# Kernel optimization log

Measured on AMD Instinct MI355X. Metric: run time of the kernel, lower is better.

## Reference

```python
import jax, jax.numpy as jnp
import numpy as np

D_MODEL = 1024
NHEAD = 16
HEAD_DIM = D_MODEL // NHEAD
FF = 4096
ALPHA = 1.4142135  # deepnorm_alpha
WIN = (127, 128)   # sliding window (left, right)
EPS = 1e-5
ROPE_BASE = 10000.0


def rmsnorm(x, g):
    ms = jnp.mean(x * x, axis=-1, keepdims=True)
    return x * jax.lax.rsqrt(ms + EPS) * g


def rope(x):
    # x: [B, T, H, D]; non-interleaved rotary over full head dim
    T, D = x.shape[1], x.shape[-1]
    half = D // 2
    inv_freq = 1.0 / (ROPE_BASE ** (jnp.arange(half, dtype=jnp.float32) * 2.0 / D))
    ang = jnp.arange(T, dtype=jnp.float32)[:, None] * inv_freq[None, :]  # [T, half]
    cos = jnp.cos(ang)[None, :, None, :]
    sin = jnp.sin(ang)[None, :, None, :]
    x1, x2 = x[..., :half], x[..., half:]
    return jnp.concatenate([x1 * cos - x2 * sin, x2 * cos + x1 * sin], axis=-1)


def setup_inputs() -> dict:
    key = jax.random.key(0)
    ks = jax.random.split(key, 8)
    d, h = D_MODEL, FF
    return {
        "x": jax.random.normal(ks[0], (2, 2048, d), jnp.float32),
        "Wqkv": jax.random.normal(ks[1], (3 * d, d), jnp.float32) * 0.02,
        "Wout": jax.random.normal(ks[2], (d, d), jnp.float32) * 0.02,
        "bout": jnp.zeros((d,), jnp.float32),
        "W1": jax.random.normal(ks[3], (2 * h, d), jnp.float32) * 0.02,
        "W2": jax.random.normal(ks[4], (d, h), jnp.float32) * 0.02,
        "g1": jnp.ones((d,), jnp.float32),
        "g2": jnp.ones((d,), jnp.float32),
    }


def reference(x, Wqkv, Wout, bout, W1, W2, g1, g2):
    B, T, d = x.shape
    # --- self attention with RoPE + sliding window band mask ---
    qkv = (x @ Wqkv.T).reshape(B, T, 3, NHEAD, HEAD_DIM)
    q, k, v = qkv[:, :, 0], qkv[:, :, 1], qkv[:, :, 2]  # [B,T,H,Dh]
    q = rope(q)
    k = rope(k)
    q = jnp.swapaxes(q, 1, 2)  # [B,H,T,Dh]
    k = jnp.swapaxes(k, 1, 2)
    v = jnp.swapaxes(v, 1, 2)
    scale = 1.0 / np.sqrt(HEAD_DIM)
    scores = jnp.einsum('bhqd,bhkd->bhqk', q, k) * scale
    idx = jnp.arange(T)
    rel = idx[None, :] - idx[:, None]  # j - i
    band = (rel >= -WIN[0]) & (rel <= WIN[1])  # [T,T] allowed positions
    scores = jnp.where(band[None, None], scores, -jnp.inf)
    attn = jax.nn.softmax(scores, axis=-1)
    o = jnp.einsum('bhqk,bhkd->bhqd', attn, v)
    o = jnp.swapaxes(o, 1, 2).reshape(B, T, d)
    a = o @ Wout.T + bout
    # --- deepnorm residual 1 + RMSNorm ---
    x1 = a + ALPHA * x
    x2 = rmsnorm(x1, g1)
    # --- SwiGLU MLP: y, gate = fc1(x).chunk(2); y*gate*sigmoid(gate) ---
    yg = x2 @ W1.T
    y, gate = jnp.split(yg, 2, axis=-1)
    y = y * gate * jax.nn.sigmoid(gate)
    y = y @ W2.T
    # --- deepnorm residual 2 + RMSNorm ---
    x3 = y + ALPHA * x2
    return rmsnorm(x3, g2)
```

## Files before the change

### kernel.cpp

```cpp
#include <hip/hip_runtime.h>

#define T_SEQ   2048
#define NHEADS  16
#define DHEAD   64
#define DMODEL  1024
#define ALPHA_C 1.4142135f
#define EPS_C   1e-5f

typedef __attribute__((ext_vector_type(8))) short bf16x8;
typedef __attribute__((ext_vector_type(4))) short bf16x4;
typedef __attribute__((ext_vector_type(4))) float floatx4;

__device__ __forceinline__ float bf2f(unsigned short u) {
  union { unsigned int i; float f; } v;
  v.i = ((unsigned int)u) << 16;
  return v.f;
}
__device__ __forceinline__ unsigned short f2bf(float f) {
  union { float f; unsigned int i; } v;
  v.f = f;
  unsigned int u = v.i;
  u += 0x7FFF + ((u >> 16) & 1);
  return (unsigned short)(u >> 16);
}

__device__ __forceinline__ void gload_lds16(const void* g, void* l) {
  __builtin_amdgcn_global_load_lds(
      (const __attribute__((address_space(1))) void*)g,
      (__attribute__((address_space(3))) void*)l, 16, 0, 0);
}

__global__ void convert_all(const float* __restrict__ Wqkv,
                            const float* __restrict__ Wout,
                            const float* __restrict__ W1,
                            const float* __restrict__ W2,
                            const float* __restrict__ x,
                            unsigned short* __restrict__ ws)
{
  size_t i = ((size_t)blockIdx.x * 256 + threadIdx.x) * 8;
  const float* src;
  size_t off;
  if      (i <  3145728) { src = Wqkv; off = i; }
  else if (i <  4194304) { src = Wout; off = i -  3145728; }
  else if (i < 12582912) { src = W1;   off = i -  4194304; }
  else if (i < 16777216) { src = W2;   off = i - 12582912; }
  else                   { src = x;    off = i - 16777216; }
  floatx4 a = *(const floatx4*)(src + off);
  floatx4 b = *(const floatx4*)(src + off + 4);
  bf16x8 o;
  #pragma unroll
  for (int u = 0; u < 4; u++) {
    o[u]     = (short)f2bf(a[u]);
    o[4 + u] = (short)f2bf(b[u]);
  }
  *(bf16x8*)(ws + i) = o;
}

__global__ void build_rope_lut(float* __restrict__ cosT,
                               float* __restrict__ sinT)
{
  int gid = blockIdx.x * 256 + threadIdx.x;
  int t = gid >> 5, i = gid & 31;
  float fr = powf(10000.f, -(float)i * (1.f / 32.f));
  float sn, cs;
  sincosf((float)t * fr, &sn, &cs);
  cosT[gid] = cs;
  sinT[gid] = sn;
}

template<int BN>
__global__ __launch_bounds__(256) void gemm_lds(
    const unsigned short* __restrict__ A,
    const unsigned short* __restrict__ W,
    unsigned short* __restrict__ C,
    const float* __restrict__ bias,
    int M, int N, int K, int lda)
{
  constexpr int WN = BN / 2;
  constexpr int NJ = WN / 16;
  __shared__ unsigned short As[128 * 32];
  __shared__ unsigned short Bs[BN * 32];

  const int tid  = threadIdx.x;
  const int lane = tid & 63;
  const int wave = tid >> 6;
  const int wm = (wave >> 1) * 64;
  const int wn = (wave & 1) * WN;
  const int mBase = blockIdx.y * 128;
  const int nBase = blockIdx.x * BN;

  const int sRow = lane >> 2;
  const int sCol = (lane & 3) * 8;

  floatx4 acc[4][NJ];
  #pragma unroll
  for (int i = 0; i < 4; i++)
    #pragma unroll
    for (int j = 0; j < NJ; j++) acc[i][j] = (floatx4){0.f, 0.f, 0.f, 0.f};

  const int mrow = lane & 15;
  const int kq   = (lane >> 4) * 8;

  for (int kb = 0; kb < K; kb += 32) {
    __syncthreads();
    #pragma unroll
    for (int j = 0; j < 2; j++) {
      int r = wave * 32 + j * 16 + sRow;
      gload_lds16(A + (size_t)(mBase + r) * lda + kb + sCol,
                  &As[wave * 1024 + j * 512 + lane * 8]);
    }
    if constexpr (BN == 128) {
      #pragma unroll
      for (int j = 0; j < 2; j++) {
        int r = wave * 32 + j * 16 + sRow;
        gload_lds16(W + (size_t)(nBase + r) * K + kb + sCol,
                    &Bs[wave * 1024 + j * 512 + lane * 8]);
      }
    } else {
      int r = wave * 16 + sRow;
      gload_lds16(W + (size_t)(nBase + r) * K + kb + sCol,
                  &Bs[wave * 512 + lane * 8]);
    }
    __syncthreads();

    bf16x8 af[4], bfr[NJ];
    #pragma unroll
    for (int i = 0; i < 4; i++)
      af[i] = *(const bf16x8*)&As[(wm + i * 16 + mrow) * 32 + kq];
    #pragma unroll
    for (int j = 0; j < NJ; j++)
      bfr[j] = *(const bf16x8*)&Bs[(wn + j * 16 + mrow) * 32 + kq];
    #pragma unroll
    for (int i = 0; i < 4; i++)
      #pragma unroll
      for (int j = 0; j < NJ; j++)
        acc[i][j] = __builtin_amdgcn_mfma_f32_16x16x32_bf16(af[i], bfr[j], acc[i][j], 0, 0, 0);
  }

  const int col0 = lane & 15;
  const int row0 = (lane >> 4) * 4;
  #pragma unroll
  for (int j = 0; j < NJ; j++) {
    const int col = nBase + wn + j * 16 + col0;
    const float badd = bias ? bias[col] : 0.f;
    #pragma unroll
    for (int i = 0; i < 4; i++) {
      #pragma unroll
      for (int r = 0; r < 4; r++) {
        const int row = mBase + wm + i * 16 + row0 + r;
        C[(size_t)row * N + col] = f2bf(acc[i][j][r] + badd);
      }
    }
  }
}

#define BAR() __builtin_amdgcn_s_barrier()
#define SCB() __builtin_amdgcn_sched_barrier(0)
#define LGKM0() do { asm volatile("s_waitcnt lgkmcnt(0)" ::: "memory"); \
                     __builtin_amdgcn_sched_barrier(0); } while (0)

#define RD_A(bb, mh)                                                      \
  _Pragma("unroll") for (int i = 0; i < 4; i++)                           \
  _Pragma("unroll") for (int s = 0; s < 2; s++)                           \
    af[i][s] = *(const bf16x8*)&lds[(bb) + aRd +                          \
        ((mh) * 64 + i * 16 + mrow) * 64 + (kq0 ^ (s << 5))];

#define RD_B(bb, nh)                                                      \
  _Pragma("unroll") for (int n = 0; n < 2; n++)                           \
  _Pragma("unroll") for (int s = 0; s < 2; s++)                           \
    bf[(nh) * 2 + n][s] = *(const bf16x8*)&lds[(bb) + bRd +               \
        (bRow0 + ((nh) * 2 + n) * 16 + mrow) * 64 + (kq0 ^ (s << 5))];

#define MFMA16(mh, nh)                                                    \
  _Pragma("unroll") for (int i = 0; i < 4; i++)                           \
  _Pragma("unroll") for (int n = 0; n < 2; n++)                           \
  _Pragma("unroll") for (int s = 0; s < 2; s++)                           \
    acc[(mh) * 4 + i][(nh) * 2 + n] =                                     \
        __builtin_amdgcn_mfma_f32_16x16x32_bf16(                          \
            af[i][s], bf[(nh) * 2 + n][s],                                \
            acc[(mh) * 4 + i][(nh) * 2 + n], 0, 0, 0);

#define KLOOP_4PH()                                                       \
  for (int t = 0; t < 16; ++t) {                                          \
    const int cur = t & 1;                                                \
    const int nxt = cur ^ 1;                                              \
    const int bb  = cur * 32768;                                          \
    const int ta  = (t + 1 < 16) ? t + 1 : 15;                            \
    const int tb  = (t + 2 < 16) ? t + 2 : 15;                            \
                                       \
    RD_A(bb, 0); RD_B(bb, 0);                                             \
    stA(nxt, 1, ta);                                                      \
    BAR(); LGKM0();                                                       \
    __builtin_amdgcn_s_setprio(1);                                        \
    MFMA16(0, 0);                                                         \
    __builtin_amdgcn_s_setprio(0);                                        \
    BAR();                                                                \
                                                     \
    RD_B(bb, 1);                                                          \
    stB(nxt, 1, ta);                                                      \
    BAR(); LGKM0();                                                       \
    __builtin_amdgcn_s_setprio(1);                                        \
    MFMA16(0, 1);                                                         \
    __builtin_amdgcn_s_setprio(0);                                        \
    BAR();                                                                \
                                                     \
    RD_A(bb, 1);                                                          \
    stB(cur, 0, tb);                                                      \
    BAR(); LGKM0();                                                       \
    __builtin_amdgcn_s_setprio(1);                                        \
    MFMA16(1, 1);                                                         \
    __builtin_amdgcn_s_setprio(0);                                        \
    BAR();                                                                \
       \
    stA(cur, 0, tb);                                                      \
    BAR(); LGKM0();                                                       \
    __builtin_amdgcn_s_setprio(1);                                        \
    MFMA16(1, 0);                                                         \
    __builtin_amdgcn_s_setprio(0);                                        \
    asm volatile("s_waitcnt vmcnt(4)" ::: "memory");                      \
    BAR();                                                                \
  }

__global__ __launch_bounds__(512, 2) void gemm_w1_swiglu_4ph(
    const unsigned short* __restrict__ A,
    const unsigned short* __restrict__ W1,
    unsigned short* __restrict__ ys)
{
  __shared__ unsigned short lds[65536];

  const int tid  = threadIdx.x;
  const int lane = tid & 63;
  const int wid  = tid >> 6;
  const int wr   = wid >> 2;
  const int wc   = wid & 3;
  const int mrow = lane & 15;
  const int quad = lane >> 4;
  const int kq0  = (quad ^ (mrow & 7)) * 8;

  const int bid  = blockIdx.x;
  const int c8   = bid & 7;
  const int u    = bid >> 3;
  const int mBase = ((c8 >> 2) * 8 + (u >> 3)) * 256;
  const int nBase = ((c8 &  3) * 8 + (u &  7)) * 128;

  const int r0 = tid >> 3;
  const int ce = (((tid & 7) ^ (r0 & 7)) * 8);
  const size_t aoff0 = (size_t)(mBase + r0) * 1024 + ce;
  const size_t aoff1 = aoff0 + (size_t)64 * 1024;
  auto growf = [&](int br) {
    int col = nBase + (br >> 6) * 32 + (br & 31);
    return ((br >> 5) & 1) ? 4096 + col : col;
  };
  const size_t boff00 = (size_t)growf(r0)       * 1024 + ce;
  const size_t boff01 = (size_t)growf(64 + r0)  * 1024 + ce;
  const size_t boff10 = (size_t)growf(128 + r0) * 1024 + ce;
  const size_t boff11 = (size_t)growf(192 + r0) * 1024 + ce;
  const int d0 = tid * 8;

  auto stA = [&](int buf, int h, int kt) {
    const unsigned short* g = A + (size_t)kt * 64 + (h ? (size_t)128 * 1024 : 0);
    int base = buf * 32768 + h * 8192;
    gload_lds16(g + aoff0, &lds[base + d0]);
    gload_lds16(g + aoff1, &lds[base + 4096 + d0]);
  };
  auto stB = [&](int buf, int h, int kt) {
    const unsigned short* g = W1 + (size_t)kt * 64;
    int base = buf * 32768 + 16384 + h * 8192;
    gload_lds16(g + (h ? boff10 : boff00), &lds[base + d0]);
    gload_lds16(g + (h ? boff11 : boff01), &lds[base + 4096 + d0]);
  };

  floatx4 acc[8][4];
  #pragma unroll
  for (int i = 0; i < 8; i++)
    #pragma unroll
    for (int n = 0; n < 4; n++) acc[i][n] = (floatx4){0.f, 0.f, 0.f, 0.f};
  bf16x8 af[4][2], bf[4][2];

  const int aRd   = wr * 8192;
  const int bRd   = 16384 + (wc >> 1) * 8192;
  const int bRow0 = (wc & 1) * 64;

  stB(0, 0, 0); stA(0, 0, 0); stA(0, 1, 0); stB(0, 1, 0);
  stB(1, 0, 1); stA(1, 0, 1);
  asm volatile("s_waitcnt vmcnt(4)" ::: "memory");
  BAR();

  KLOOP_4PH();

  const int col0 = lane & 15;
  const int row0 = (lane >> 4) * 4;
  #pragma unroll
  for (int n = 0; n < 2; n++) {
    const int col = nBase + wc * 32 + n * 16 + col0;
    #pragma unroll
    for (int i = 0; i < 8; i++) {
      const int rowb = mBase + wr * 128 + i * 16 + row0;
      #pragma unroll
      for (int r = 0; r < 4; r++) {
        float y = acc[i][n][r], g = acc[i][n + 2][r];
        float sig = 1.f / (1.f + __expf(-g));
        ys[(size_t)(rowb + r) * 4096 + col] = f2bf(y * g * sig);
      }
    }
  }
  asm volatile("s_waitcnt vmcnt(0)" ::: "memory");
}

__global__ __launch_bounds__(512, 2) void gemm_qkv_rope256(
    const unsigned short* __restrict__ A,
    const unsigned short* __restrict__ W,
    const float* __restrict__ cosT,
    const float* __restrict__ sinT,
    unsigned short* __restrict__ Qd,
    unsigned short* __restrict__ Kd,
    unsigned short* __restrict__ Vd)
{
  __shared__ unsigned short lds[65536];

  const int tid  = threadIdx.x;
  const int lane = tid & 63;
  const int wid  = tid >> 6;
  const int wr   = wid >> 2;
  const int wc   = wid & 3;
  const int mrow = lane & 15;
  const int quad = lane >> 4;
  const int kq0  = (quad ^ (mrow & 7)) * 8;

  const int bid  = blockIdx.x;
  const int c8   = bid & 7;
  const int u    = bid >> 3;
  const int mBase = ((c8 >> 1) * 4 + u / 6) * 256;
  const int nBase = ((c8 & 1) * 6 + u % 6) * 256;

  const int r0 = tid >> 3;
  const int ce = (((tid & 7) ^ (r0 & 7)) * 8);
  const size_t aoff0 = (size_t)(mBase + r0) * 1024 + ce;
  const size_t aoff1 = aoff0 + (size_t)64 * 1024;
  const size_t boff00 = (size_t)(nBase + r0)       * 1024 + ce;
  const size_t boff01 = (size_t)(nBase + 64 + r0)  * 1024 + ce;
  const size_t boff10 = (size_t)(nBase + 128 + r0) * 1024 + ce;
  const size_t boff11 = (size_t)(nBase + 192 + r0) * 1024 + ce;
  const int d0 = tid * 8;

  auto stA = [&](int buf, int h, int kt) {
    const unsigned short* g = A + (size_t)kt * 64 + (h ? (size_t)128 * 1024 : 0);
    int base = buf * 32768 + h * 8192;
    gload_lds16(g + aoff0, &lds[base + d0]);
    gload_lds16(g + aoff1, &lds[base + 4096 + d0]);
  };
  auto stB = [&](int buf, int h, int kt) {
    const unsigned short* g = W + (size_t)kt * 64;
    int base = buf * 32768 + 16384 + h * 8192;
    gload_lds16(g + (h ? boff10 : boff00), &lds[base + d0]);
    gload_lds16(g + (h ? boff11 : boff01), &lds[base + 4096 + d0]);
  };

  floatx4 acc[8][4];
  #pragma unroll
  for (int i = 0; i < 8; i++)
    #pragma unroll
    for (int n = 0; n < 4; n++) acc[i][n] = (floatx4){0.f, 0.f, 0.f, 0.f};
  bf16x8 af[4][2], bf[4][2];

  const int aRd   = wr * 8192;
  const int bRd   = 16384 + (wc >> 1) * 8192;
  const int bRow0 = (wc & 1) * 64;

  stB(0, 0, 0); stA(0, 0, 0); stA(0, 1, 0); stB(0, 1, 0);
  stB(1, 0, 1); stA(1, 0, 1);
  asm volatile("s_waitcnt vmcnt(4)" ::: "memory");
  BAR();

  KLOOP_4PH();

  const int col0 = lane & 15;
  const int row0 = (lane >> 4) * 4;
  const int colBase = nBase + wc * 64;
  const int sect = colBase >> 10;
  const int h    = (colBase & 1023) >> 6;
  unsigned short* dst = (sect == 0) ? Qd : (sect == 1) ? Kd : Vd;

  if (sect < 2) {
    #pragma unroll
    for (int i = 0; i < 8; i++) {
      #pragma unroll
      for (int r = 0; r < 4; r++) {
        const int row = mBase + wr * 128 + i * 16 + row0 + r;
        const int b = row >> 11, t = row & 2047;
        size_t ob = ((size_t)((b * NHEADS + h) * T_SEQ + t)) * DHEAD;
        const int tb = t * 32;
        float c0 = cosT[tb + col0],      s0 = sinT[tb + col0];
        float c1 = cosT[tb + col0 + 16], s1 = sinT[tb + col0 + 16];
        float x1a = acc[i][0][r], x2a = acc[i][2][r];
        float x1b = acc[i][1][r], x2b = acc[i][3][r];
        dst[ob + col0]      = f2bf(x1a * c0 - x2a * s0);
        dst[ob + col0 + 32] = f2bf(x2a * c0 + x1a * s0);
        dst[ob + col0 + 16] = f2bf(x1b * c1 - x2b * s1);
        dst[ob + col0 + 48] = f2bf(x2b * c1 + x1b * s1);
      }
    }
  } else {
    #pragma unroll
    for (int i = 0; i < 8; i++)
      #pragma unroll
      for (int n = 0; n < 4; n++)
        #pragma unroll
        for (int r = 0; r < 4; r++) {
          const int row = mBase + wr * 128 + i * 16 + row0 + r;
          const int b = row >> 11, t = row & 2047;
          dst[((size_t)((b * NHEADS + h) * T_SEQ + t)) * DHEAD + n * 16 + col0] =
              f2bf(acc[i][n][r]);
        }
  }
  asm volatile("s_waitcnt vmcnt(0)" ::: "memory");
}

#define W2_RD_A(bb, mh, s)                                                \
  _Pragma("unroll") for (int i = 0; i < 2; i++)                           \
    af[i][s] = *(const bf16x8*)&lds[(bb) +                                \
        (wr * 64 + (mh) * 32 + i * 16 + mrow) * 64 + (kq0 ^ ((s) << 5))];

#define W2_RD_B(bb, s)                                                    \
  _Pragma("unroll") for (int n = 0; n < 4; n++)                           \
    bfr[n][s] = *(const bf16x8*)&lds[(bb) + 16384 +                       \
        (wc * 64 + n * 16 + mrow) * 64 + (kq0 ^ ((s) << 5))];

#define W2_MFMA(mh, s)                                                    \
  _Pragma("unroll") for (int i = 0; i < 2; i++)                           \
  _Pragma("unroll") for (int n = 0; n < 4; n++)                           \
    acc[(mh) * 2 + i][n] =                                                \
        __builtin_amdgcn_mfma_f32_16x16x32_bf16(                          \
            af[i][s], bfr[n][s], acc[(mh) * 2 + i][n], 0, 0, 0);

__global__ __launch_bounds__(512, 2) void gemm_w2_2ph(
    const unsigned short* __restrict__ A,
    const unsigned short* __restrict__ W,
    float* __restrict__ Cp)
{
  __shared__ unsigned short lds[49152];

  const int tid  = threadIdx.x;
  const int lane = tid & 63;
  const int wid  = tid >> 6;
  const int wr   = wid >> 1;
  const int wc   = wid & 1;
  const int mrow = lane & 15;
  const int quad = lane >> 4;
  const int kq0  = (quad ^ (mrow & 7)) * 8;

  const int u  = blockIdx.x;
  const int c8 = u & 7;
  const int v  = u >> 3;
  const int zP = v >> 4;
  const int mBase = (((c8 >> 1) & 3) * 4 + ((v >> 2) & 3)) * 256;
  const int nBase = ((c8 & 1) * 4 + (v & 3)) * 128;
  const int kOff  = zP * 2048;

  const int r0 = tid >> 3;
  const int ce = (((tid & 7) ^ (r0 & 7)) * 8);
  const int d0 = tid * 8;

  auto stA = [&](int buf, int h, int kt) {
    const unsigned short* g =
        A + (size_t)(mBase + h * 128 + r0) * 4096 + kOff + kt * 64 + ce;
    int base = buf * 24576 + h * 8192;
    gload_lds16(g, &lds[base + d0]);
    gload_lds16(g + (size_t)64 * 4096, &lds[base + 4096 + d0]);
  };
  auto stB = [&](int buf, int kt) {
    const unsigned short* g =
        W + (size_t)(nBase + r0) * 4096 + kOff + kt * 64 + ce;
    int base = buf * 24576 + 16384;
    gload_lds16(g, &lds[base + d0]);
    gload_lds16(g + (size_t)64 * 4096, &lds[base + 4096 + d0]);
  };

  floatx4 acc[4][4];
  #pragma unroll
  for (int i = 0; i < 4; i++)
    #pragma unroll
    for (int n = 0; n < 4; n++) acc[i][n] = (floatx4){0.f, 0.f, 0.f, 0.f};
  bf16x8 af[2][2], bfr[4][2];

  stB(0, 0);
  stA(0, 0, 0); stA(0, 1, 0);
  stB(1, 1);
  asm volatile("s_waitcnt vmcnt(2)" ::: "memory");

  for (int t = 0; t < 32; ++t) {
    const int cur = t & 1;
    const int nxt = cur ^ 1;
    const int bb  = cur * 24576;
    const int ta  = (t + 1 < 32) ? t + 1 : 31;
    const int tb  = (t + 2 < 32) ? t + 2 : 31;

    BAR();
    stA(nxt, 0, ta); stA(nxt, 1, ta);
    W2_RD_A(bb, 0, 0); W2_RD_B(bb, 0);
    SCB();
    W2_RD_A(bb, 0, 1); W2_RD_B(bb, 1);
    asm volatile("s_waitcnt lgkmcnt(6)" ::: "memory");
    SCB();
    __builtin_amdgcn_s_setprio(1);
    W2_MFMA(0, 0);
    __builtin_amdgcn_s_setprio(0);
    asm volatile("s_waitcnt lgkmcnt(0)" ::: "memory");
    SCB();
    __builtin_amdgcn_s_setprio(1);
    W2_MFMA(0, 1);
    __builtin_amdgcn_s_setprio(0);

    BAR();
    stB(cur, tb);
    W2_RD_A(bb, 1, 0);
    SCB();
    W2_RD_A(bb, 1, 1);
    asm volatile("s_waitcnt lgkmcnt(2)" ::: "memory");
    SCB();
    __builtin_amdgcn_s_setprio(1);
    W2_MFMA(1, 0);
    __builtin_amdgcn_s_setprio(0);
    asm volatile("s_waitcnt lgkmcnt(0)" ::: "memory");
    SCB();
    __builtin_amdgcn_s_setprio(1);
    W2_MFMA(1, 1);
    __builtin_amdgcn_s_setprio(0);
    asm volatile("s_waitcnt vmcnt(2)" ::: "memory");
  }

  const int col0 = lane & 15;
  const int row0 = (lane >> 4) * 4;
  float* dst = Cp + (size_t)zP * 4096 * 1024;
  #pragma unroll
  for (int n = 0; n < 4; n++) {
    const int col = nBase + wc * 64 + n * 16 + col0;
    #pragma unroll
    for (int i = 0; i < 4; i++) {
      const int rowb = mBase + wr * 64 + i * 16 + row0;
      #pragma unroll
      for (int r = 0; r < 4; r++)
        dst[(size_t)(rowb + r) * 1024 + col] = acc[i][n][r];
    }
  }
  asm volatile("s_waitcnt vmcnt(0)" ::: "memory");
}

__global__ __launch_bounds__(256) void attn_mfma(
    const unsigned short* __restrict__ Qg,
    const unsigned short* __restrict__ Kg,
    const unsigned short* __restrict__ Vg,
    unsigned short* __restrict__ Og)
{
  __shared__ unsigned short KV[23040];
  __shared__ unsigned short Qs[64 * 72];
  __shared__ unsigned short Ps[4 * 16 * 328];

  const int tid  = threadIdx.x;
  const int lane = tid & 63;
  const int wave = tid >> 6;
  const int c    = lane & 15;
  const int quad = lane >> 4;
  const int blk  = blockIdx.x;
  const int bh   = blk >> 5;
  const int qBase = (blk & 31) * 64;
  const size_t hbase = (size_t)bh * T_SEQ * DHEAD;

  for (int e = tid; e < 320 * 8; e += 256) {
    int row = e >> 3, ch = e & 7;
    int kg = qBase - 127 + row;
    int kgc = min(max(kg, 0), T_SEQ - 1);
    *(bf16x8*)&KV[row * 72 + ch * 8] =
        *(const bf16x8*)(Kg + hbase + (size_t)kgc * DHEAD + ch * 8);
  }
  for (int e = tid; e < 64 * 8; e += 256) {
    int row = e >> 3, ch = e & 7;
    *(bf16x8*)&Qs[row * 72 + ch * 8] =
        *(const bf16x8*)(Qg + hbase + (size_t)(qBase + row) * DHEAD + ch * 8);
  }
  __syncthreads();

  bf16x8 aq[2];
  #pragma unroll
  for (int hh = 0; hh < 2; hh++)
    aq[hh] = *(const bf16x8*)&Qs[(wave * 16 + c) * 72 + hh * 32 + quad * 8];

  floatx4 s[20];
  #pragma unroll
  for (int kt = 0; kt < 20; kt++) {
    bf16x8 b0 = *(const bf16x8*)&KV[(kt * 16 + c) * 72 + quad * 8];
    bf16x8 b1 = *(const bf16x8*)&KV[(kt * 16 + c) * 72 + 32 + quad * 8];
    floatx4 t = (floatx4){0.f, 0.f, 0.f, 0.f};
    t = __builtin_amdgcn_mfma_f32_16x16x32_bf16(aq[0], b0, t, 0, 0, 0);
    t = __builtin_amdgcn_mfma_f32_16x16x32_bf16(aq[1], b1, t, 0, 0, 0);
    s[kt] = t;
  }
  __syncthreads();

  for (int ch = wave; ch < 5; ch += 4) {
    int koff = ch * 64 + lane;
    int kg = qBase - 127 + koff;
    int kgc = min(max(kg, 0), T_SEQ - 1);
    const unsigned short* vrow = Vg + hbase + (size_t)kgc * DHEAD;
    #pragma unroll
    for (int dg = 0; dg < 8; dg++) {
      bf16x8 v8 = *(const bf16x8*)(vrow + dg * 8);
      #pragma unroll
      for (int j = 0; j < 8; j++)
        KV[(dg * 8 + j) * 328 + koff] = (unsigned short)v8[j];
    }
  }

  const int kLoMin = max(0, 127 - qBase);
  const int kHiMax = min(319, 2047 + 127 - qBase);
  float mx[4] = {-3e38f, -3e38f, -3e38f, -3e38f};
  #pragma unroll
  for (int kt = 0; kt < 20; kt++) {
    const int koff = kt * 16 + c;
    #pragma unroll
    for (int reg = 0; reg < 4; reg++) {
      const int qrow = wave * 16 + quad * 4 + reg;
      const int d = koff - qrow;
      bool ok = (d >= 0) && (d <= 255) && (koff >= kLoMin) && (koff <= kHiMax);
      float val = ok ? s[kt][reg] * 0.125f : -3e38f;
      s[kt][reg] = val;
      mx[reg] = fmaxf(mx[reg], val);
    }
  }
  #pragma unroll
  for (int reg = 0; reg < 4; reg++)
    #pragma unroll
    for (int m = 1; m <= 8; m <<= 1)
      mx[reg] = fmaxf(mx[reg], __shfl_xor(mx[reg], m));

  float ls[4] = {0.f, 0.f, 0.f, 0.f};
  #pragma unroll
  for (int kt = 0; kt < 20; kt++) {
    const int koff = kt * 16 + c;
    #pragma unroll
    for (int reg = 0; reg < 4; reg++) {
      float p = __expf(s[kt][reg] - mx[reg]);
      ls[reg] += p;
      Ps[wave * 5248 + (quad * 4 + reg) * 328 + koff] = f2bf(p);
    }
  }
  float inv[4];
  #pragma unroll
  for (int reg = 0; reg < 4; reg++) {
    #pragma unroll
    for (int m = 1; m <= 8; m <<= 1) ls[reg] += __shfl_xor(ls[reg], m);
    inv[reg] = 1.f / ls[reg];
  }
  __syncthreads();

  floatx4 oacc[4];
  #pragma unroll
  for (int nt = 0; nt < 4; nt++) oacc[nt] = (floatx4){0.f, 0.f, 0.f, 0.f};
  #pragma unroll
  for (int kt2 = 0; kt2 < 10; kt2++) {
    bf16x8 a = *(const bf16x8*)&Ps[wave * 5248 + c * 328 + kt2 * 32 + quad * 8];
    #pragma unroll
    for (int nt = 0; nt < 4; nt++) {
      bf16x8 bb = *(const bf16x8*)&KV[(nt * 16 + c) * 328 + kt2 * 32 + quad * 8];
      oacc[nt] = __builtin_amdgcn_mfma_f32_16x16x32_bf16(a, bb, oacc[nt], 0, 0, 0);
    }
  }

  const int b = bh >> 4, h = bh & 15;
  #pragma unroll
  for (int nt = 0; nt < 4; nt++) {
    #pragma unroll
    for (int reg = 0; reg < 4; reg++) {
      const int qg = qBase + wave * 16 + quad * 4 + reg;
      Og[((size_t)(b * T_SEQ + qg)) * DMODEL + h * DHEAD + nt * 16 + c] =
          f2bf(oacc[nt][reg] * inv[reg]);
    }
  }
}

__global__ __launch_bounds__(256) void rmsnorm_mid(
    const unsigned short* __restrict__ a,
    const float* __restrict__ x,
    const float* __restrict__ g,
    unsigned short* __restrict__ out)
{
  __shared__ float red[4];
  const int row = blockIdx.x;
  const int tid = threadIdx.x;
  const size_t base = (size_t)row * DMODEL;
  const int c = tid * 4;
  bf16x4  av = *(const bf16x4*)(a + base + c);
  floatx4 xv = *(const floatx4*)(x + base + c);
  floatx4 gv = *(const floatx4*)(g + c);
  float s[4], ss = 0.f;
  #pragma unroll
  for (int j = 0; j < 4; j++) {
    s[j] = bf2f((unsigned short)av[j]) + ALPHA_C * xv[j];
    ss += s[j] * s[j];
  }
  #pragma unroll
  for (int m = 1; m <= 32; m <<= 1) ss += __shfl_xor(ss, m);
  if ((tid & 63) == 0) red[tid >> 6] = ss;
  __syncthreads();
  float ms = (red[0] + red[1] + red[2] + red[3]) * (1.f / DMODEL);
  float scl = rsqrtf(ms + EPS_C);
  bf16x4 ov;
  #pragma unroll
  for (int j = 0; j < 4; j++) ov[j] = (short)f2bf(s[j] * scl * gv[j]);
  *(bf16x4*)(out + base + c) = ov;
}

__global__ __launch_bounds__(256) void rmsnorm_final_sk(
    const float* __restrict__ p0,
    const float* __restrict__ p1,
    const unsigned short* __restrict__ x2,
    const float* __restrict__ g,
    float* __restrict__ out)
{
  __shared__ float red[4];
  const int row = blockIdx.x;
  const int tid = threadIdx.x;
  const size_t base = (size_t)row * DMODEL;
  const int c = tid * 4;
  floatx4 a0 = *(const floatx4*)(p0 + base + c);
  floatx4 a1 = *(const floatx4*)(p1 + base + c);
  bf16x4  xv = *(const bf16x4*)(x2 + base + c);
  floatx4 gv = *(const floatx4*)(g + c);
  float s[4], ss = 0.f;
  #pragma unroll
  for (int j = 0; j < 4; j++) {
    s[j] = (a0[j] + a1[j]) + ALPHA_C * bf2f((unsigned short)xv[j]);
    ss += s[j] * s[j];
  }
  #pragma unroll
  for (int m = 1; m <= 32; m <<= 1) ss += __shfl_xor(ss, m);
  if ((tid & 63) == 0) red[tid >> 6] = ss;
  __syncthreads();
  float ms = (red[0] + red[1] + red[2] + red[3]) * (1.f / DMODEL);
  float scl = rsqrtf(ms + EPS_C);
  floatx4 ov;
  #pragma unroll
  for (int j = 0; j < 4; j++) ov[j] = s[j] * scl * gv[j];
  *(floatx4*)(out + base + c) = ov;
}

extern "C" void kernel_launch(void* const* d_in, const int* in_sizes, int n_in,
                              void* d_out, int out_size, void* d_ws, size_t ws_size,
                              hipStream_t stream) {
  (void)in_sizes; (void)n_in; (void)out_size; (void)ws_size;
  const float* x    = (const float*)d_in[0];
  const float* Wqkv = (const float*)d_in[1];
  const float* Wout = (const float*)d_in[2];
  const float* bout = (const float*)d_in[3];
  const float* W1   = (const float*)d_in[4];
  const float* W2   = (const float*)d_in[5];
  const float* g1   = (const float*)d_in[6];
  const float* g2   = (const float*)d_in[7];
  float* out = (float*)d_out;

  unsigned short* ws    = (unsigned short*)d_ws;
  unsigned short* Wqkvb = ws;
  unsigned short* Woutb = ws + 3145728;
  unsigned short* W1b   = ws + 4194304;
  unsigned short* W2b   = ws + 12582912;
  unsigned short* P1    = ws + 16777216;
  unsigned short* x2    = ws + 20971520;
  unsigned short* q     = ws + 25165824;
  unsigned short* k     = ws + 29360128;
  unsigned short* v     = ws + 33554432;
  unsigned short* o     = ws + 37748736;
  unsigned short* ys    = ws + 25165824;
  float* cosT = (float*)(ws + 37748736);
  float* sinT = cosT + 65536;
  float* p0   = (float*)(ws + 41943040);

  build_rope_lut<<<256, 256, 0, stream>>>(cosT, sinT);
  convert_all<<<10240, 256, 0, stream>>>(Wqkv, Wout, W1, W2, x, ws);
  gemm_qkv_rope256<<<192, 512, 0, stream>>>(P1, Wqkvb, cosT, sinT, q, k, v);
  attn_mfma<<<32 * (T_SEQ / 64), 256, 0, stream>>>(q, k, v, o);
  gemm_lds<64><<<dim3(16, 32), 256, 0, stream>>>(o, Woutb, P1, bout, 4096, 1024, 1024, 1024);
  rmsnorm_mid<<<4096, 256, 0, stream>>>(P1, x, g1, x2);
  gemm_w1_swiglu_4ph<<<512, 512, 0, stream>>>(x2, W1b, ys);
  gemm_w2_2ph<<<256, 512, 0, stream>>>(ys, W2b, p0);
  rmsnorm_final_sk<<<4096, 256, 0, stream>>>(p0, p0 + 4194304, x2, g2, out);
}
```

Baseline: 346.6 us.

## Restructure 4-phase GEMM k-loop with split LDS reads and fewer barriers; fuse RoPE LUT build

The big GEMM k-loop (used by the W1/SwiGLU kernel and the QKV kernel) is reorganised. LDS fragment reads are split by k-half, and partial lgkmcnt waits let the first half of the MFMAs start while the second half is still loading. The B fragments for both n-halves are loaded up front, which removes two of the LDS read phases and roughly halves the barriers per iteration, at the cost of more live registers. The RoPE cos/sin table build is folded into extra blocks of the weight-convert kernel, saving one kernel launch.

```diff
diff --git a/kernel.cpp b/kernel.cpp
--- a/kernel.cpp
+++ b/kernel.cpp
@@ -35,8 +35,20 @@
                             const float* __restrict__ W1,
                             const float* __restrict__ W2,
                             const float* __restrict__ x,
-                            unsigned short* __restrict__ ws)
+                            unsigned short* __restrict__ ws,
+                            float* __restrict__ cosT,
+                            float* __restrict__ sinT)
 {
+  if (blockIdx.x >= 10240) {
+    int gid = (blockIdx.x - 10240) * 256 + threadIdx.x;
+    int t = gid >> 5, i = gid & 31;
+    float fr = powf(10000.f, -(float)i * (1.f / 32.f));
+    float sn, cs;
+    sincosf((float)t * fr, &sn, &cs);
+    cosT[gid] = cs;
+    sinT[gid] = sn;
+    return;
+  }
   size_t i = ((size_t)blockIdx.x * 256 + threadIdx.x) * 8;
   const float* src;
   size_t off;
@@ -54,18 +66,6 @@
     o[4 + u] = (short)f2bf(b[u]);
   }
   *(bf16x8*)(ws + i) = o;
-}
-
-__global__ void build_rope_lut(float* __restrict__ cosT,
-                               float* __restrict__ sinT)
-{
-  int gid = blockIdx.x * 256 + threadIdx.x;
-  int t = gid >> 5, i = gid & 31;
-  float fr = powf(10000.f, -(float)i * (1.f / 32.f));
-  float sn, cs;
-  sincosf((float)t * fr, &sn, &cs);
-  cosT[gid] = cs;
-  sinT[gid] = sn;
 }
 
 template<int BN>
@@ -156,72 +156,80 @@
 
 #define BAR() __builtin_amdgcn_s_barrier()
 #define SCB() __builtin_amdgcn_sched_barrier(0)
-#define LGKM0() do { asm volatile("s_waitcnt lgkmcnt(0)" ::: "memory"); \
-                     __builtin_amdgcn_sched_barrier(0); } while (0)
-
-#define RD_A(bb, mh)                                                      \
+
+#define RD_A_S(bb, mh, s)                                                 \
   _Pragma("unroll") for (int i = 0; i < 4; i++)                           \
-  _Pragma("unroll") for (int s = 0; s < 2; s++)                           \
     af[i][s] = *(const bf16x8*)&lds[(bb) + aRd +                          \
-        ((mh) * 64 + i * 16 + mrow) * 64 + (kq0 ^ (s << 5))];
-
-#define RD_B(bb, nh)                                                      \
-  _Pragma("unroll") for (int n = 0; n < 2; n++)                           \
-  _Pragma("unroll") for (int s = 0; s < 2; s++)                           \
-    bf[(nh) * 2 + n][s] = *(const bf16x8*)&lds[(bb) + bRd +               \
-        (bRow0 + ((nh) * 2 + n) * 16 + mrow) * 64 + (kq0 ^ (s << 5))];
-
-#define MFMA16(mh, nh)                                                    \
+        ((mh) * 64 + i * 16 + mrow) * 64 + (kq0 ^ ((s) << 5))];
+
+#define RD_B_S(bb, s)                                                     \
+  _Pragma("unroll") for (int n = 0; n < 4; n++)                           \
+    bfr[n][s] = *(const bf16x8*)&lds[(bb) + bRd +                         \
+        (bRow0 + n * 16 + mrow) * 64 + (kq0 ^ ((s) << 5))];
+
+#define MFMA8(mh, nh, s)                                                  \
   _Pragma("unroll") for (int i = 0; i < 4; i++)                           \
   _Pragma("unroll") for (int n = 0; n < 2; n++)                           \
-  _Pragma("unroll") for (int s = 0; s < 2; s++)                           \
     acc[(mh) * 4 + i][(nh) * 2 + n] =                                     \
         __builtin_amdgcn_mfma_f32_16x16x32_bf16(                          \
-            af[i][s], bf[(nh) * 2 + n][s],                                \
+            af[i][s], bfr[(nh) * 2 + n][s],                               \
             acc[(mh) * 4 + i][(nh) * 2 + n], 0, 0, 0);
 
-#define KLOOP_4PH()                                                       \
+#define KLOOP_S4()                                                        \
   for (int t = 0; t < 16; ++t) {                                          \
     const int cur = t & 1;                                                \
     const int nxt = cur ^ 1;                                              \
     const int bb  = cur * 32768;                                          \
     const int ta  = (t + 1 < 16) ? t + 1 : 15;                            \
     const int tb  = (t + 2 < 16) ? t + 2 : 15;                            \
-                                       \
-    RD_A(bb, 0); RD_B(bb, 0);                                             \
+                                                             \
+    BAR();                                                                \
     stA(nxt, 1, ta);                                                      \
-    BAR(); LGKM0();                                                       \
+    RD_A_S(bb, 0, 0); RD_B_S(bb, 0);                                      \
+    SCB();                                                                \
+    RD_A_S(bb, 0, 1); RD_B_S(bb, 1);                                      \
+    asm volatile("s_waitcnt lgkmcnt(8)" ::: "memory");                    \
+    SCB();                                                                \
     __builtin_amdgcn_s_setprio(1);                                        \
-    MFMA16(0, 0);                                                         \
+    MFMA8(0, 0, 0);                                                       \
     __builtin_amdgcn_s_setprio(0);                                        \
+    asm volatile("s_waitcnt lgkmcnt(0)" ::: "memory");                    \
+    SCB();                                                                \
+    __builtin_amdgcn_s_setprio(1);                                        \
+    MFMA8(0, 0, 1);                                                       \
+    __builtin_amdgcn_s_setprio(0);                                        \
+                                                             \
     BAR();                                                                \
-                                                     \
-    RD_B(bb, 1);                                                          \
     stB(nxt, 1, ta);                                                      \
-    BAR(); LGKM0();                                                       \
     __builtin_amdgcn_s_setprio(1);                                        \
-    MFMA16(0, 1);                                                         \
+    MFMA8(0, 1, 0); MFMA8(0, 1, 1);                                       \
     __builtin_amdgcn_s_setprio(0);                                        \
+                                                             \
     BAR();                                                                \
-                                                     \
-    RD_A(bb, 1);                                                          \
     stB(cur, 0, tb);                                                      \
-    BAR(); LGKM0();                                                       \
+    RD_A_S(bb, 1, 0);                                                     \
+    SCB();                                                                \
+    RD_A_S(bb, 1, 1);                                                     \
+    asm volatile("s_waitcnt lgkmcnt(4)" ::: "memory");                    \
+    SCB();                                                                \
     __builtin_amdgcn_s_setprio(1);                                        \
-    MFMA16(1, 1);                                                         \
+    MFMA8(1, 1, 0);                                                       \
     __builtin_amdgcn_s_setprio(0);                                        \
+    asm volatile("s_waitcnt lgkmcnt(0)" ::: "memory");                    \
+    SCB();                                                                \
+    __builtin_amdgcn_s_setprio(1);                                        \
+    MFMA8(1, 1, 1);                                                       \
+    __builtin_amdgcn_s_setprio(0);                                        \
+                                                             \
     BAR();                                                                \
-       \
     stA(cur, 0, tb);                                                      \
-    BAR(); LGKM0();                                                       \
     __builtin_amdgcn_s_setprio(1);                                        \
-    MFMA16(1, 0);                                                         \
+    MFMA8(1, 0, 0); MFMA8(1, 0, 1);                                       \
     __builtin_amdgcn_s_setprio(0);                                        \
     asm volatile("s_waitcnt vmcnt(4)" ::: "memory");                      \
-    BAR();                                                                \
-  }
-
-__global__ __launch_bounds__(512, 2) void gemm_w1_swiglu_4ph(
+  }
+
+__global__ __launch_bounds__(512, 2) void gemm_w1_swiglu_s4(
     const unsigned short* __restrict__ A,
     const unsigned short* __restrict__ W1,
     unsigned short* __restrict__ ys)
@@ -275,7 +283,7 @@
   for (int i = 0; i < 8; i++)
     #pragma unroll
     for (int n = 0; n < 4; n++) acc[i][n] = (floatx4){0.f, 0.f, 0.f, 0.f};
-  bf16x8 af[4][2], bf[4][2];
+  bf16x8 af[4][2], bfr[4][2];
 
   const int aRd   = wr * 8192;
   const int bRd   = 16384 + (wc >> 1) * 8192;
@@ -284,9 +292,8 @@
   stB(0, 0, 0); stA(0, 0, 0); stA(0, 1, 0); stB(0, 1, 0);
   stB(1, 0, 1); stA(1, 0, 1);
   asm volatile("s_waitcnt vmcnt(4)" ::: "memory");
-  BAR();
-
-  KLOOP_4PH();
+
+  KLOOP_S4();
 
   const int col0 = lane & 15;
   const int row0 = (lane >> 4) * 4;
@@ -361,7 +368,7 @@
   for (int i = 0; i < 8; i++)
     #pragma unroll
     for (int n = 0; n < 4; n++) acc[i][n] = (floatx4){0.f, 0.f, 0.f, 0.f};
-  bf16x8 af[4][2], bf[4][2];
+  bf16x8 af[4][2], bfr[4][2];
 
   const int aRd   = wr * 8192;
   const int bRd   = 16384 + (wc >> 1) * 8192;
@@ -370,9 +377,8 @@
   stB(0, 0, 0); stA(0, 0, 0); stA(0, 1, 0); stB(0, 1, 0);
   stB(1, 0, 1); stA(1, 0, 1);
   asm volatile("s_waitcnt vmcnt(4)" ::: "memory");
-  BAR();
-
-  KLOOP_4PH();
+
+  KLOOP_S4();
 
   const int col0 = lane & 15;
   const int row0 = (lane >> 4) * 4;
@@ -774,13 +780,12 @@
   float* sinT = cosT + 65536;
   float* p0   = (float*)(ws + 41943040);
 
-  build_rope_lut<<<256, 256, 0, stream>>>(cosT, sinT);
-  convert_all<<<10240, 256, 0, stream>>>(Wqkv, Wout, W1, W2, x, ws);
+  convert_all<<<10496, 256, 0, stream>>>(Wqkv, Wout, W1, W2, x, ws, cosT, sinT);
   gemm_qkv_rope256<<<192, 512, 0, stream>>>(P1, Wqkvb, cosT, sinT, q, k, v);
   attn_mfma<<<32 * (T_SEQ / 64), 256, 0, stream>>>(q, k, v, o);
   gemm_lds<64><<<dim3(16, 32), 256, 0, stream>>>(o, Woutb, P1, bout, 4096, 1024, 1024, 1024);
   rmsnorm_mid<<<4096, 256, 0, stream>>>(P1, x, g1, x2);
-  gemm_w1_swiglu_4ph<<<512, 512, 0, stream>>>(x2, W1b, ys);
+  gemm_w1_swiglu_s4<<<512, 512, 0, stream>>>(x2, W1b, ys);
   gemm_w2_2ph<<<256, 512, 0, stream>>>(ys, W2b, p0);
   rmsnorm_final_sk<<<4096, 256, 0, stream>>>(p0, p0 + 4194304, x2, g2, out);
 }
```

After: 350.0 us. About the same (+1.0%).
